# Optimization experiments

Hardware: AMD Instinct MI355X
Metric: run time of the kernel (lower is better)

Reference implementation:

```python
import jax, jax.numpy as jnp
import numpy as np
from jax import lax

B, NCH, T = 256, 32, 2000
NTF, NSF, NSUB, TK = 4, 40, 20, 25
NCLS = 4
NTAN = NSUB * (NSUB + 1) // 2
REIG_EPS = 1e-4


def setup_inputs() -> dict:
    key = jax.random.key(0)
    ks = jax.random.split(key, 8)
    x = jax.random.normal(ks[0], (B, NCH, T), dtype=jnp.float32)
    conv1_w = jax.random.normal(ks[1], (NTF, 1, 1, TK), dtype=jnp.float32) * 0.2
    conv1_b = jnp.zeros((NTF,), dtype=jnp.float32)
    conv2_w = jax.random.normal(ks[2], (NSF, NTF, NCH, 1), dtype=jnp.float32) * 0.1
    conv2_b = jnp.zeros((NSF,), dtype=jnp.float32)
    # BiMap weight: semi-orthogonal (n_subspace x n_spatial_filters) via QR
    A = jax.random.normal(ks[3], (NSF, NSUB), dtype=jnp.float32)
    Q, _ = jnp.linalg.qr(A)
    W_bimap = Q.T  # (NSUB, NSF), rows orthonormal
    clf_w = jax.random.normal(ks[4], (NCLS, NTAN), dtype=jnp.float32) * 0.05
    clf_b = jnp.zeros((NCLS,), dtype=jnp.float32)
    return {"x": x, "conv1_w": conv1_w, "conv1_b": conv1_b,
            "conv2_w": conv2_w, "conv2_b": conv2_b,
            "W_bimap": W_bimap, "clf_w": clf_w, "clf_b": clf_b}


def _forward(x, conv1_w, conv1_b, conv2_w, conv2_b, W_bimap, clf_w, clf_b):
    dn = ('NCHW', 'OIHW', 'NCHW')
    h = x[:, None, :, :]  # (B,1,NCH,T)
    # temporal conv, 'same' with reflect padding along time
    pl = (TK - 1) // 2
    pr = TK - 1 - pl
    hp = jnp.pad(h, ((0, 0), (0, 0), (0, 0), (pl, pr)), mode='reflect')
    h1 = lax.conv_general_dilated(hp, conv1_w, (1, 1), 'VALID', dimension_numbers=dn)
    h1 = h1 + conv1_b[None, :, None, None]  # (B,NTF,NCH,T)
    # spatial conv collapses channel axis
    h2 = lax.conv_general_dilated(h1, conv2_w, (1, 1), 'VALID', dimension_numbers=dn)
    h2 = h2 + conv2_b[None, :, None, None]  # (B,NSF,1,T)
    h2 = h2.reshape(B, NSF, T)
    # covariance pooling over time (unbiased)
    hm = h2 - h2.mean(axis=-1, keepdims=True)
    C = jnp.einsum('bft,bgt->bfg', hm, hm) / (T - 1)  # (B,NSF,NSF)
    # BiMap: S = W C W^T  -> (B,NSUB,NSUB)
    S = jnp.einsum('if,bfg,jg->bij', W_bimap, C, W_bimap)
    # ReEig: clamp eigenvalues at threshold
    w, U = jnp.linalg.eigh(S)
    w = jnp.maximum(w, REIG_EPS)
    S = jnp.einsum('bik,bk,bjk->bij', U, w, U)
    # LogEig: matrix log, take scaled upper triangle, flatten
    w2, U2 = jnp.linalg.eigh(S)
    L = jnp.einsum('bik,bk,bjk->bij', U2, jnp.log(w2), U2)
    iu, ju = jnp.triu_indices(NSUB)
    scale = jnp.where(iu == ju, 1.0, jnp.sqrt(2.0)).astype(L.dtype)
    z = L[:, iu, ju] * scale[None, :]  # (B, NTAN)
    return z @ clf_w.T + clf_b


def reference(x, conv1_w, conv1_b, conv2_w, conv2_b, W_bimap, clf_w, clf_b):
    return _forward(x, conv1_w, conv1_b, conv2_w, conv2_b, W_bimap, clf_w, clf_b)
```

## Files before the change

### kernel.cpp

```cpp
#include <hip/hip_runtime.h>
#include <math.h>

#define B_    256
#define NCH   32
#define T_    2000
#define NTF   4
#define NSF   40
#define NSUB  20
#define TK    25
#define NCLS  4
#define NTAN  210
#define NPAIR 820
#define ACC_STRIDE 860
#define TILE_T 250
#define NTILE  8
#define PL     12

#define ACC_FLOATS (B_*ACC_STRIDE)
#define W2Q_OFF ACC_FLOATS
#define W1T_OFF (W2Q_OFF + NSF*NTF*NCH)
#define CB_OFF  (W1T_OFF + NTF*TK)

#define XS_TSTR 36
#define H2_STR  256
#define H2_CHK  63
#define LDS_DW  10240

typedef float v2f __attribute__((ext_vector_type(2)));
typedef float v4f __attribute__((ext_vector_type(4)));

__device__ __forceinline__ v2f fma2(v2f a, v2f b, v2f c) {
#if __has_builtin(__builtin_elementwise_fma)
    return __builtin_elementwise_fma(a, b, c);
#else
    v2f r; r.x = fmaf(a.x, b.x, c.x); r.y = fmaf(a.y, b.y, c.y); return r;
#endif
}

__device__ __forceinline__ v4f fma4(v4f a, v4f b, v4f c) {
#if __has_builtin(__builtin_elementwise_fma)
    return __builtin_elementwise_fma(a, b, c);
#else
    v4f r;
    r.x = fmaf(a.x, b.x, c.x); r.y = fmaf(a.y, b.y, c.y);
    r.z = fmaf(a.z, b.z, c.z); r.w = fmaf(a.w, b.w, c.w);
    return r;
#endif
}

__device__ __forceinline__ int pack_ut(int f, int g) {
    return f*NSF - (f*(f-1))/2 + (g - f);
}

__global__ void prep_kernel(const float* __restrict__ conv1_w,
                            const float* __restrict__ conv1_b,
                            const float* __restrict__ conv2_w,
                            const float* __restrict__ conv2_b,
                            float* __restrict__ ws) {
    int tid = threadIdx.x;
    for (int i = blockIdx.x*256 + tid; i < ACC_FLOATS; i += 256*256) ws[i] = 0.f;
    if (blockIdx.x != 0) return;

    float* w2q = ws + W2Q_OFF;
    float* w1t = ws + W1T_OFF;
    float* cb  = ws + CB_OFF;
    for (int i = tid; i < NSF*NTF*NCH; i += 256) {
        int j  = i & 3;
        int q  = i >> 2;
        int s4 = q % 10;
        int cf = q / 10;
        int f  = cf & 3;
        int c  = cf >> 2;
        int s  = 4*s4 + j;
        w2q[i] = conv2_w[(s*NTF + f)*NCH + c];
    }
    for (int i = tid; i < NTF*TK; i += 256) {
        int f = i & 3;
        int k = i >> 2;
        w1t[i] = conv1_w[f*TK + k];
    }
    if (tid < NSF) {
        float s = conv2_b[tid];
        #pragma unroll
        for (int f = 0; f < NTF; ++f) {
            float a = 0.f;
            for (int c = 0; c < NCH; ++c) a += conv2_w[(tid*NTF + f)*NCH + c];
            s = fmaf(a, conv1_b[f], s);
        }
        cb[tid] = s;
    }
}

__global__ __launch_bounds__(256, 4)
void conv_gram_kernel(const float* __restrict__ x,
                      const float* __restrict__ wts,
                      float* __restrict__ acc)
{
    __shared__ float lds[LDS_DW];

    const int tid  = threadIdx.x;
    const int bid  = blockIdx.x;
    const int b    = bid >> 3;
    const int tile = bid & 7;
    const int t0   = tile * TILE_T;

    const float* xb = x + (size_t)b*NCH*T_;
    for (int li = tid; li < NCH*280; li += 256) {
        int c = li / 280;
        int i = li - c*280;
        int tg = t0 + i - PL;
        tg = (tg < 0) ? -tg : tg;
        tg = (tg >= T_) ? (2*T_ - 2 - tg) : tg;
        lds[i*XS_TSTR + c] = xb[c*T_ + tg];
    }
    __syncthreads();

    const float4* w1t = (const float4*)(wts + W1T_OFF);
    const float4* w2q = (const float4*)(wts + W2Q_OFF);
    const float4* cb4 = (const float4*)(wts + CB_OFF);

    v4f acc4[10];
    #pragma unroll
    for (int s4 = 0; s4 < 10; ++s4) {
        float4 t = cb4[s4];
        v4f a; a.x = t.x; a.y = t.y; a.z = t.z; a.w = t.w;
        acc4[s4] = a;
    }

    #pragma clang loop unroll(disable)
    for (int ch = 0; ch < 4; ++ch) {
        v2f h1[16];
        #pragma unroll
        for (int i = 0; i < 16; ++i) h1[i] = (v2f)0.f;

        #pragma clang loop unroll(disable)
        for (int k = 0; k < TK; ++k) {
            float4 wq = w1t[k];
            v2f w01; w01.x = wq.x; w01.y = wq.y;
            v2f w23; w23.x = wq.z; w23.y = wq.w;
            const float4* xr = (const float4*)&lds[(tid + k)*XS_TSTR + 8*ch];
            float4 xa = xr[0];
            float4 xb4 = xr[1];
            float xv[8] = {xa.x, xa.y, xa.z, xa.w, xb4.x, xb4.y, xb4.z, xb4.w};
            #pragma unroll
            for (int c = 0; c < 8; ++c) {
                v2f xc; xc.x = xv[c]; xc.y = xv[c];
                h1[2*c]   = fma2(xc, w01, h1[2*c]);
                h1[2*c+1] = fma2(xc, w23, h1[2*c+1]);
            }
        }

        const float4* wp = w2q + (ch*8)*(NTF*10);
        #pragma unroll
        for (int c = 0; c < 8; ++c) {
            float hf[4] = {h1[2*c].x, h1[2*c].y, h1[2*c+1].x, h1[2*c+1].y};
            #pragma unroll
            for (int f = 0; f < 4; ++f) {
                v4f hb; hb.x = hf[f]; hb.y = hf[f]; hb.z = hf[f]; hb.w = hf[f];
                #pragma unroll
                for (int s4 = 0; s4 < 10; ++s4) {
                    float4 w = wp[(c*4 + f)*10 + s4];
                    v4f wv; wv.x = w.x; wv.y = w.y; wv.z = w.z; wv.w = w.w;
                    acc4[s4] = fma4(hb, wv, acc4[s4]);
                }
            }
        }
    }
    __syncthreads();

    if (tid < 252) {
        const bool valid = (tid < TILE_T);
        const int qw = tid >> 2;
        const int ew = tid & 3;
        #pragma unroll
        for (int s4 = 0; s4 < 10; ++s4) {
            v4f a = acc4[s4];
            const int col = (((qw ^ (s4 & 7)) << 2) | ew);
            lds[(4*s4+0)*H2_STR + col] = valid ? a.x : 0.f;
            lds[(4*s4+1)*H2_STR + col] = valid ? a.y : 0.f;
            lds[(4*s4+2)*H2_STR + col] = valid ? a.z : 0.f;
            lds[(4*s4+3)*H2_STR + col] = valid ? a.w : 0.f;
        }
    }
    __syncthreads();

    float* accb = acc + b*ACC_STRIDE;

    if (tid < 55) {
        int bf = 0, rem = tid;
        while (rem >= 10 - bf) { rem -= 10 - bf; bf++; }
        int bg = bf + rem;
        const int xa = bf & 7;
        const int xbq = bg & 7;

        const float4* rA[4];
        const float4* rB[4];
        #pragma unroll
        for (int a = 0; a < 4; ++a) {
            rA[a] = (const float4*)&lds[(4*bf + a)*H2_STR];
            rB[a] = (const float4*)&lds[(4*bg + a)*H2_STR];
        }
        v2f accL[16], accH[16];
        #pragma unroll
        for (int i = 0; i < 16; ++i) { accL[i] = (v2f)0.f; accH[i] = (v2f)0.f; }

        #pragma unroll 7
        for (int q = 0; q < H2_CHK; ++q) {
            float4 av[4], bv[4];
            #pragma unroll
            for (int a = 0; a < 4; ++a) av[a] = rA[a][q ^ xa];
            #pragma unroll
            for (int a = 0; a < 4; ++a) bv[a] = rB[a][q ^ xbq];
            #pragma unroll
            for (int a = 0; a < 4; ++a) {
                v2f aL; aL.x = av[a].x; aL.y = av[a].y;
                v2f aH; aH.x = av[a].z; aH.y = av[a].w;
                #pragma unroll
                for (int g = 0; g < 4; ++g) {
                    v2f bL; bL.x = bv[g].x; bL.y = bv[g].y;
                    v2f bH; bH.x = bv[g].z; bH.y = bv[g].w;
                    accL[a*4+g] = fma2(aL, bL, accL[a*4+g]);
                    accH[a*4+g] = fma2(aH, bH, accH[a*4+g]);
                }
            }
        }
        #pragma unroll
        for (int a = 0; a < 4; ++a) {
            #pragma unroll
            for (int g = 0; g < 4; ++g) {
                int f  = 4*bf + a;
                int gg = 4*bg + g;
                if (f <= gg) {
                    v2f sL = accL[a*4+g], sH = accH[a*4+g];
                    float s = (sL.x + sL.y) + (sH.x + sH.y);
                    atomicAdd(&accb[pack_ut(f, gg)], s);
                }
            }
        }
    }

    if (tid >= 64 && tid < 64 + NSF) {
        int row = tid - 64;
        const int xr = (row >> 2) & 7;
        const float4* rr = (const float4*)&lds[row*H2_STR];
        float csum = 0.f;
        #pragma unroll 7
        for (int q = 0; q < H2_CHK; ++q) {
            float4 v = rr[q ^ xr];
            csum += (v.x + v.y) + (v.z + v.w);
        }
        atomicAdd(&accb[NPAIR + row], csum);
    }
}

__device__ __forceinline__ void pq_sched(int r, int k, int& p, int& q) {
    if (k == 0) { p = 19; q = r; }
    else {
        int a = r + k;      if (a >= 19) a -= 19;
        int d = r - k + 19; if (d >= 19) d -= 19;
        p = a; q = d;
    }
}

__global__ __launch_bounds__(128)
void finalize_kernel(const float* __restrict__ acc,
                     const float* __restrict__ W_bimap,
                     const float* __restrict__ clf_w,
                     const float* __restrict__ clf_b,
                     float* __restrict__ out)
{
    __shared__ float C[NSF*NSF];
    __shared__ float Wb[NSUB*NSF];
    __shared__ float M[NSUB*NSF];
    __shared__ float A[NSUB*21];
    __shared__ float V[NSUB*21];
    __shared__ float cs_c[10], cs_s[10];
    __shared__ float lam[NSUB];
    __shared__ float z[NTAN];

    const int tid = threadIdx.x;
    const int b   = blockIdx.x;
    const float* accb = acc + b*ACC_STRIDE;

    for (int i = tid; i < NSF*NSF; i += 128) {
        int f = i / NSF, g = i % NSF;
        int lo = f < g ? f : g;
        int hi = f < g ? g : f;
        double G  = (double)accb[pack_ut(lo, hi)];
        double sf = (double)accb[NPAIR + f];
        double sg = (double)accb[NPAIR + g];
        C[i] = (float)((G - sf*sg/(double)T_) / (double)(T_ - 1));
    }
    for (int i = tid; i < NSUB*NSF; i += 128) Wb[i] = W_bimap[i];
    __syncthreads();

    for (int i = tid; i < NSUB*NSF; i += 128) {
        int r = i / NSF, g = i % NSF;
        float s = 0.f;
        #pragma unroll 8
        for (int f = 0; f < NSF; ++f) s = fmaf(Wb[r*NSF+f], C[f*NSF+g], s);
        M[i] = s;
    }
    __syncthreads();

    for (int i = tid; i < NSUB*NSUB; i += 128) {
        int r = i / NSUB, j = i % NSUB;
        float s = 0.f;
        #pragma unroll 8
        for (int g = 0; g < NSF; ++g) s = fmaf(M[r*NSF+g], Wb[j*NSF+g], s);
        A[r*21+j] = s;
        V[r*21+j] = (r == j) ? 1.f : 0.f;
    }
    __syncthreads();

    const int kk = tid / 10;
    const int ll = tid - 10*(tid/10);

    for (int sweep = 0; sweep < 7; ++sweep) {
        for (int r = 0; r < 19; ++r) {
            if (tid < 10) {
                int p, q; pq_sched(r, tid, p, q);
                float app = A[p*21+p], aqq = A[q*21+q], apq = A[p*21+q];
                float c = 1.f, s = 0.f;
                if (fabsf(apq) > 1e-30f) {
                    float tau = (aqq - app) / (2.f*apq);
                    float t = 1.f / (fabsf(tau) + sqrtf(1.f + tau*tau));
                    if (tau < 0.f) t = -t;
                    c = 1.f / sqrtf(1.f + t*t);
                    s = t * c;
                }
                cs_c[tid] = c; cs_s[tid] = s;
            }
            __syncthreads();
            if (tid < 100) {
                int pk, qk, pl, ql;
                pq_sched(r, kk, pk, qk);
                pq_sched(r, ll, pl, ql);
                float ck = cs_c[kk], sk = cs_s[kk];
                float cl = cs_c[ll], sl = cs_s[ll];
                float a00 = A[pk*21+pl], a01 = A[pk*21+ql];
                float a10 = A[qk*21+pl], a11 = A[qk*21+ql];
                float t00 = ck*a00 - sk*a10, t01 = ck*a01 - sk*a11;
                float t10 = sk*a00 + ck*a10, t11 = sk*a01 + ck*a11;
                A[pk*21+pl] = cl*t00 - sl*t01;
                A[pk*21+ql] = sl*t00 + cl*t01;
                A[qk*21+pl] = cl*t10 - sl*t11;
                A[qk*21+ql] = sl*t10 + cl*t11;
                float v00 = V[pk*21+pl], v01 = V[pk*21+ql];
                float v10 = V[qk*21+pl], v11 = V[qk*21+ql];
                V[pk*21+pl] = cl*v00 - sl*v01;
                V[pk*21+ql] = sl*v00 + cl*v01;
                V[qk*21+pl] = cl*v10 - sl*v11;
                V[qk*21+ql] = sl*v10 + cl*v11;
            }
            __syncthreads();
        }
    }

    if (tid < NSUB) {
        float w = A[tid*21+tid];
        lam[tid] = logf(fmaxf(w, 1e-4f));
    }
    __syncthreads();

    for (int p = tid; p < NTAN; p += 128) {
        int i = 0, rem = p;
        while (rem >= NSUB - i) { rem -= NSUB - i; i++; }
        int j = i + rem;
        float s = 0.f;
        #pragma unroll 5
        for (int k = 0; k < NSUB; ++k) s = fmaf(V[i*21+k]*lam[k], V[j*21+k], s);
        z[p] = (i == j) ? s : s * 1.41421356237309515f;
    }
    __syncthreads();

    if (tid < NCLS) {
        float s = clf_b[tid];
        for (int p = 0; p < NTAN; ++p) s = fmaf(clf_w[tid*NTAN+p], z[p], s);
        out[b*NCLS + tid] = s;
    }
}

extern "C" void kernel_launch(void* const* d_in, const int* in_sizes, int n_in,
                              void* d_out, int out_size, void* d_ws, size_t ws_size,
                              hipStream_t stream) {
    const float* x       = (const float*)d_in[0];
    const float* conv1_w = (const float*)d_in[1];
    const float* conv1_b = (const float*)d_in[2];
    const float* conv2_w = (const float*)d_in[3];
    const float* conv2_b = (const float*)d_in[4];
    const float* W_bimap = (const float*)d_in[5];
    const float* clf_w   = (const float*)d_in[6];
    const float* clf_b   = (const float*)d_in[7];
    float* out = (float*)d_out;
    float* ws  = (float*)d_ws;

    prep_kernel<<<256, 256, 0, stream>>>(conv1_w, conv1_b, conv2_w, conv2_b, ws);
    conv_gram_kernel<<<B_*NTILE, 256, 0, stream>>>(x, ws, ws);
    finalize_kernel<<<B_, 128, 0, stream>>>(ws, W_bimap, clf_w, clf_b, out);
}
```

Measured before the change: 337.4 us.

## Run Jacobi eigen sweeps in a single wavefront with shuffles instead of barriers

The parallel Jacobi eigensolver in the finalize kernel now runs on one 64-lane wavefront. Rotation coefficients are broadcast with __shfl instead of shared memory, and each lane handles up to two of the 100 2x2 block updates. This removes the two block-wide __syncthreads per rotation round (7x19 rounds) and relies on wavefront lockstep execution for ordering between the coefficient read and the LDS update. The trade-off is less parallelism per round and an implicit assumption that wave64 LDS accesses stay ordered without explicit barriers.

```diff
diff --git a/kernel.cpp b/kernel.cpp
--- a/kernel.cpp
+++ b/kernel.cpp
@@ -274,7 +274,6 @@
     __shared__ float M[NSUB*NSF];
     __shared__ float A[NSUB*21];
     __shared__ float V[NSUB*21];
-    __shared__ float cs_c[10], cs_s[10];
     __shared__ float lam[NSUB];
     __shared__ float z[NTAN];
 
@@ -313,49 +312,78 @@
     }
     __syncthreads();
 
-    const int kk = tid / 10;
-    const int ll = tid - 10*(tid/10);
-
-    for (int sweep = 0; sweep < 7; ++sweep) {
-        for (int r = 0; r < 19; ++r) {
-            if (tid < 10) {
-                int p, q; pq_sched(r, tid, p, q);
-                float app = A[p*21+p], aqq = A[q*21+q], apq = A[p*21+q];
-                float c = 1.f, s = 0.f;
-                if (fabsf(apq) > 1e-30f) {
-                    float tau = (aqq - app) / (2.f*apq);
-                    float t = 1.f / (fabsf(tau) + sqrtf(1.f + tau*tau));
-                    if (tau < 0.f) t = -t;
-                    c = 1.f / sqrtf(1.f + t*t);
-                    s = t * c;
-                }
-                cs_c[tid] = c; cs_s[tid] = s;
+    if (tid < 64) {
+        const int kk1 = tid / 10;
+        const int ll1 = tid - 10*kk1;
+        const int i2  = tid + 64;
+        const bool has2 = (tid < 36);
+        const int kk2 = i2 / 10;
+        const int ll2 = i2 - 10*kk2;
+        const int kk2c = has2 ? kk2 : 0;
+
+        for (int sweep = 0; sweep < 7; ++sweep) {
+            for (int r = 0; r < 19; ++r) {
+                float c_own = 1.f, s_own = 0.f;
+                if (tid < 10) {
+                    int p, q; pq_sched(r, tid, p, q);
+                    float app = A[p*21+p], aqq = A[q*21+q], apq = A[p*21+q];
+                    if (fabsf(apq) > 1e-30f) {
+                        float tau = (aqq - app) / (2.f*apq);
+                        float t = 1.f / (fabsf(tau) + sqrtf(1.f + tau*tau));
+                        if (tau < 0.f) t = -t;
+                        c_own = 1.f / sqrtf(1.f + t*t);
+                        s_own = t * c_own;
+                    }
+                }
+                float ck1 = __shfl(c_own, kk1), sk1 = __shfl(s_own, kk1);
+                float cl1 = __shfl(c_own, ll1), sl1 = __shfl(s_own, ll1);
+                float ck2 = __shfl(c_own, kk2c), sk2 = __shfl(s_own, kk2c);
+                float cl2 = __shfl(c_own, ll2),  sl2 = __shfl(s_own, ll2);
+
+                int pk1,qk1,pl1,ql1; pq_sched(r, kk1, pk1, qk1); pq_sched(r, ll1, pl1, ql1);
+                float a00 = A[pk1*21+pl1], a01 = A[pk1*21+ql1];
+                float a10 = A[qk1*21+pl1], a11 = A[qk1*21+ql1];
+                float v00 = V[pk1*21+pl1], v01 = V[pk1*21+ql1];
+                float v10 = V[qk1*21+pl1], v11 = V[qk1*21+ql1];
+
+                int pk2=0,qk2=0,pl2=0,ql2=0;
+                float b00=0.f,b01=0.f,b10=0.f,b11=0.f,w00=0.f,w01=0.f,w10=0.f,w11=0.f;
+                if (has2) {
+                    pq_sched(r, kk2, pk2, qk2); pq_sched(r, ll2, pl2, ql2);
+                    b00 = A[pk2*21+pl2]; b01 = A[pk2*21+ql2];
+                    b10 = A[qk2*21+pl2]; b11 = A[qk2*21+ql2];
+                    w00 = V[pk2*21+pl2]; w01 = V[pk2*21+ql2];
+                    w10 = V[qk2*21+pl2]; w11 = V[qk2*21+ql2];
+                }
+
+                {
+                    float t00 = ck1*a00 - sk1*a10, t01 = ck1*a01 - sk1*a11;
+                    float t10 = sk1*a00 + ck1*a10, t11 = sk1*a01 + ck1*a11;
+                    A[pk1*21+pl1] = cl1*t00 - sl1*t01;
+                    A[pk1*21+ql1] = sl1*t00 + cl1*t01;
+                    A[qk1*21+pl1] = cl1*t10 - sl1*t11;
+                    A[qk1*21+ql1] = sl1*t10 + cl1*t11;
+                    V[pk1*21+pl1] = cl1*v00 - sl1*v01;
+                    V[pk1*21+ql1] = sl1*v00 + cl1*v01;
+                    V[qk1*21+pl1] = cl1*v10 - sl1*v11;
+                    V[qk1*21+ql1] = sl1*v10 + cl1*v11;
+                }
+                if (has2) {
+                    float t00 = ck2*b00 - sk2*b10, t01 = ck2*b01 - sk2*b11;
+                    float t10 = sk2*b00 + ck2*b10, t11 = sk2*b01 + ck2*b11;
+                    A[pk2*21+pl2] = cl2*t00 - sl2*t01;
+                    A[pk2*21+ql2] = sl2*t00 + cl2*t01;
+                    A[qk2*21+pl2] = cl2*t10 - sl2*t11;
+                    A[qk2*21+ql2] = sl2*t10 + cl2*t11;
+                    V[pk2*21+pl2] = cl2*w00 - sl2*w01;
+                    V[pk2*21+ql2] = sl2*w00 + cl2*w01;
+                    V[qk2*21+pl2] = cl2*w10 - sl2*w11;
+                    V[qk2*21+ql2] = sl2*w10 + cl2*w11;
+                }
             }
-            __syncthreads();
-            if (tid < 100) {
-                int pk, qk, pl, ql;
-                pq_sched(r, kk, pk, qk);
-                pq_sched(r, ll, pl, ql);
-                float ck = cs_c[kk], sk = cs_s[kk];
-                float cl = cs_c[ll], sl = cs_s[ll];
-                float a00 = A[pk*21+pl], a01 = A[pk*21+ql];
-                float a10 = A[qk*21+pl], a11 = A[qk*21+ql];
-                float t00 = ck*a00 - sk*a10, t01 = ck*a01 - sk*a11;
-                float t10 = sk*a00 + ck*a10, t11 = sk*a01 + ck*a11;
-                A[pk*21+pl] = cl*t00 - sl*t01;
-                A[pk*21+ql] = sl*t00 + cl*t01;
-                A[qk*21+pl] = cl*t10 - sl*t11;
-                A[qk*21+ql] = sl*t10 + cl*t11;
-                float v00 = V[pk*21+pl], v01 = V[pk*21+ql];
-                float v10 = V[qk*21+pl], v11 = V[qk*21+ql];
-                V[pk*21+pl] = cl*v00 - sl*v01;
-                V[pk*21+ql] = sl*v00 + cl*v01;
-                V[qk*21+pl] = cl*v10 - sl*v11;
-                V[qk*21+ql] = sl*v10 + cl*v11;
-            }
-            __syncthreads();
-        }
-    }
+        }
+    }
+    __syncthreads();
 
     if (tid < NSUB) {
         float w = A[tid*21+tid];
```

Result: slower. 353.1 us (+4.6%).
